# Optimization experiments

Hardware: AMD Instinct MI355X
Metric: run time of the kernel (lower is better)

## Reference

```python
import jax, jax.numpy as jnp
import numpy as np

B, NX, NY, T = 8, 512, 512, 2_000_000


def setup_inputs() -> dict:
    key = jax.random.key(0)
    k1, k2, k3 = jax.random.split(key, 3)
    # regular source grid (flattened row-major: flat = j*NX + i, x varies fastest)
    xs = jnp.linspace(0.0, 1.0, NX, dtype=jnp.float32)
    ys = jnp.linspace(0.0, 1.0, NY, dtype=jnp.float32)
    SX, SY = jnp.meshgrid(xs, ys)  # (NY, NX)
    src_x = SX.reshape(1, -1)
    src_y = SY.reshape(1, -1)
    # target points strictly inside the convex hull (no NaN extrapolation)
    eps = 1e-3
    tgt_x = jax.random.uniform(k1, (1, T), jnp.float32, eps, 1.0 - eps)
    tgt_y = jax.random.uniform(k2, (1, T), jnp.float32, eps, 1.0 - eps)
    x = jax.random.normal(k3, (B, NX * NY, 1), jnp.float32)
    return {"x": x, "src_x": src_x, "src_y": src_y,
            "tgt_x": tgt_x, "tgt_y": tgt_y, "nx": NX, "ny": NY}


def reference(x, src_x, src_y, tgt_x, tgt_y, nx, ny):
    # Linear ND (triangulated) interpolation of x from a regular source grid
    # onto scattered target points. Each grid cell is split along the
    # (i,j)-(i+1,j+1) diagonal; barycentric weights inside each triangle.
    sx = src_x.reshape(-1)
    sy = src_y.reshape(-1)
    tx = tgt_x.reshape(-1)
    ty = tgt_y.reshape(-1)
    x0, x1 = sx.min(), sx.max()
    y0, y1 = sy.min(), sy.max()
    dx = (x1 - x0) / (nx - 1)
    dy = (y1 - y0) / (ny - 1)
    fx = (tx - x0) / dx
    fy = (ty - y0) / dy
    ix = jnp.clip(jnp.floor(fx), 0, nx - 2)
    iy = jnp.clip(jnp.floor(fy), 0, ny - 2)
    u = fx - ix  # local cell coords in [0,1]
    v = fy - iy
    ii = jax.lax.stop_gradient(ix).astype(jnp.int32)
    jj = jax.lax.stop_gradient(iy).astype(jnp.int32)
    base = jj * nx + ii
    i00, i10, i01, i11 = base, base + 1, base + nx, base + nx + 1
    lower = (u + v) <= 1.0  # which triangle of the cell
    idx = jnp.where(lower[:, None],
                    jnp.stack([i00, i10, i01], axis=-1),
                    jnp.stack([i11, i10, i01], axis=-1))  # [t,3]
    w = jnp.where(lower[:, None],
                  jnp.stack([1.0 - u - v, u, v], axis=-1),
                  jnp.stack([u + v - 1.0, 1.0 - v, 1.0 - u], axis=-1))  # [t,3]
    vals = x[:, idx, 0]                      # [b,t,3] gather of triangle vertices
    out = jnp.einsum('btk,tk->bt', vals, w)  # barycentric combination
    return out[..., None]                    # [b,t,1]
```

## Files before the change

### kernel.cpp

```cpp
#include <hip/hip_runtime.h>
#include <hip/hip_fp16.h>


typedef float  f32x4 __attribute__((ext_vector_type(4)));
typedef unsigned int u32x4 __attribute__((ext_vector_type(4)));

__device__ __forceinline__ unsigned pack_h2(float lo, float hi) {
    union { __half2 h2; unsigned u; } cv;
    cv.h2 = __float22half2_rn(make_float2(lo, hi));
    return cv.u;
}

__global__ __launch_bounds__(256) void build_grid16(
    const float* __restrict__ x,
    u32x4* __restrict__ rec,
    int N)
{
    const int p0 = (blockIdx.x * blockDim.x + threadIdx.x) * 4;
    if (p0 + 4 <= N) {
        f32x4 v[8];
        #pragma unroll
        for (int b = 0; b < 8; ++b)
            v[b] = *reinterpret_cast<const f32x4*>(x + (long)b * N + p0);
        #pragma unroll
        for (int k = 0; k < 4; ++k) {
            u32x4 r;
            r[0] = pack_h2(v[0][k], v[1][k]);
            r[1] = pack_h2(v[2][k], v[3][k]);
            r[2] = pack_h2(v[4][k], v[5][k]);
            r[3] = pack_h2(v[6][k], v[7][k]);
            rec[p0 + k] = r;
        }
    } else {
        for (int p = p0; p < N; ++p) {
            u32x4 r;
            r[0] = pack_h2(x[p], x[(long)N + p]);
            r[1] = pack_h2(x[2L * N + p], x[3L * N + p]);
            r[2] = pack_h2(x[4L * N + p], x[5L * N + p]);
            r[3] = pack_h2(x[6L * N + p], x[7L * N + p]);
            rec[p] = r;
        }
    }
}

__device__ __forceinline__ void half8_to_float8(u32x4 u, float* f) {
    union { u32x4 v; __half2 h2[4]; } cv;
    cv.v = u;
    float2 a = __half22float2(cv.h2[0]); f[0] = a.x; f[1] = a.y;
    float2 b = __half22float2(cv.h2[1]); f[2] = b.x; f[3] = b.y;
    float2 c = __half22float2(cv.h2[2]); f[4] = c.x; f[5] = c.y;
    float2 d = __half22float2(cv.h2[3]); f[6] = d.x; f[7] = d.y;
}

#define TPT 4

#define LOAD_TGT(c, tx, ty) do {                                          \
    const int _t0 = (c) * TPT;                                            \
    tx = __builtin_nontemporal_load(                                      \
        reinterpret_cast<const f32x4*>(tgt_x + _t0));                     \
    ty = __builtin_nontemporal_load(                                      \
        reinterpret_cast<const f32x4*>(tgt_y + _t0));                     \
} while (0)

#define GATHER(tx, ty, w0, w1, w2, r0, r1, r2) do {                       \
    _Pragma("unroll")                                                     \
    for (int k = 0; k < TPT; ++k) {                                       \
        float fx = (tx[k] - x0) * rdx;                                    \
        float fy = (ty[k] - y0) * rdy;                                    \
        float ix = fminf(fmaxf(floorf(fx), 0.0f), ixmax);                 \
        float iy = fminf(fmaxf(floorf(fy), 0.0f), iymax);                 \
        float u = fx - ix;                                                \
        float v = fy - iy;                                                \
        bool lower = (u + v) <= 1.0f;                                     \
        int g = (int)iy * nx + (int)ix;                                   \
        w0[k] = lower ? (1.0f - u - v) : (u + v - 1.0f);                  \
        w1[k] = lower ? u : (1.0f - v);                                   \
        w2[k] = lower ? v : (1.0f - u);                                   \
        r0[k] = rec[g + (lower ? 0 : (nx + 1))];                          \
        r1[k] = rec[g + 1];                                               \
        r2[k] = rec[g + nx];                                              \
    }                                                                     \
} while (0)

#define CONSUME(c, w0, w1, w2, r0, r1, r2) do {                           \
    const int _t0 = (c) * TPT;                                            \
    float res[TPT][8];                                                    \
    _Pragma("unroll")                                                     \
    for (int k = 0; k < TPT; ++k) {                                       \
        float f0[8], f1[8], f2[8];                                        \
        half8_to_float8(r0[k], f0);                                       \
        half8_to_float8(r1[k], f1);                                       \
        half8_to_float8(r2[k], f2);                                       \
        _Pragma("unroll")                                                 \
        for (int b = 0; b < 8; ++b)                                       \
            res[k][b] = f0[b] * w0[k] + f1[b] * w1[k] + f2[b] * w2[k];    \
    }                                                                     \
    _Pragma("unroll")                                                     \
    for (int b = 0; b < 8; ++b) {                                         \
        f32x4 r4 = { res[0][b], res[1][b], res[2][b], res[3][b] };        \
        __builtin_nontemporal_store(                                      \
            r4, reinterpret_cast<f32x4*>(out + (long)b * T + _t0));       \
    }                                                                     \
} while (0)

__global__ __launch_bounds__(256, 2) void interp_pipe_kernel(
    const u32x4* __restrict__ rec,
    const float* __restrict__ src_x,
    const float* __restrict__ src_y,
    const float* __restrict__ tgt_x,
    const float* __restrict__ tgt_y,
    const int* __restrict__ nx_p,
    float* __restrict__ out,
    int T, int N)
{
    const int nx = *nx_p;
    const int ny = N / nx;
    const float x0 = src_x[0];
    const float x1 = src_x[nx - 1];
    const float y0 = src_y[0];
    const float y1 = src_y[N - 1];
    const float rdx = (float)(nx - 1) / (x1 - x0);
    const float rdy = (float)(ny - 1) / (y1 - y0);
    const float ixmax = (float)(nx - 2);
    const float iymax = (float)(ny - 2);

    const int nch = T / TPT;
    const int gsz = gridDim.x * blockDim.x;
    const int tid = blockIdx.x * blockDim.x + threadIdx.x;

    {
        const int tail0 = nch * TPT;
        if (tid < T - tail0) {
            const int t = tail0 + tid;
            float fx = (tgt_x[t] - x0) * rdx;
            float fy = (tgt_y[t] - y0) * rdy;
            float ix = fminf(fmaxf(floorf(fx), 0.0f), ixmax);
            float iy = fminf(fmaxf(floorf(fy), 0.0f), iymax);
            float u = fx - ix;
            float v = fy - iy;
            bool lower = (u + v) <= 1.0f;
            int g = (int)iy * nx + (int)ix;
            u32x4 q0 = rec[g + (lower ? 0 : (nx + 1))];
            u32x4 q1 = rec[g + 1];
            u32x4 q2 = rec[g + nx];
            float w0 = lower ? (1.0f - u - v) : (u + v - 1.0f);
            float w1 = lower ? u : (1.0f - v);
            float w2 = lower ? v : (1.0f - u);
            float f0[8], f1[8], f2[8];
            half8_to_float8(q0, f0);
            half8_to_float8(q1, f1);
            half8_to_float8(q2, f2);
            for (int b = 0; b < 8; ++b)
                out[(long)b * T + t] = f0[b] * w0 + f1[b] * w1 + f2[b] * w2;
        }
    }

    int cCur = tid;
    if (cCur >= nch) return;
    int cNxt = cCur + gsz;
    int cPre = cNxt + gsz;

    f32x4 txA, tyA, txB, tyB;
    float wA0[TPT], wA1[TPT], wA2[TPT];
    float wB0[TPT], wB1[TPT], wB2[TPT];
    u32x4 rA0[TPT], rA1[TPT], rA2[TPT];
    u32x4 rB0[TPT], rB1[TPT], rB2[TPT];

    LOAD_TGT(cCur, txA, tyA);
    bool haveNxt = (cNxt < nch);
    if (haveNxt) LOAD_TGT(cNxt, txB, tyB);
    GATHER(txA, tyA, wA0, wA1, wA2, rA0, rA1, rA2);

    while (true) {
        if (!haveNxt) { CONSUME(cCur, wA0, wA1, wA2, rA0, rA1, rA2); break; }
        if (cPre < nch) LOAD_TGT(cPre, txA, tyA);
        GATHER(txB, tyB, wB0, wB1, wB2, rB0, rB1, rB2);
        CONSUME(cCur, wA0, wA1, wA2, rA0, rA1, rA2);
        cCur = cNxt; cNxt = cPre; cPre += gsz;
        haveNxt = (cNxt < nch);
        if (!haveNxt) { CONSUME(cCur, wB0, wB1, wB2, rB0, rB1, rB2); break; }
        if (cPre < nch) LOAD_TGT(cPre, txB, tyB);
        GATHER(txA, tyA, wA0, wA1, wA2, rA0, rA1, rA2);
        CONSUME(cCur, wB0, wB1, wB2, rB0, rB1, rB2);
        cCur = cNxt; cNxt = cPre; cPre += gsz;
        haveNxt = (cNxt < nch);
    }
}

__global__ __launch_bounds__(256) void interp_fallback_kernel(
    const float* __restrict__ x,
    const float* __restrict__ src_x,
    const float* __restrict__ src_y,
    const float* __restrict__ tgt_x,
    const float* __restrict__ tgt_y,
    const int* __restrict__ nx_p,
    float* __restrict__ out,
    int T, int N, int B)
{
    const int nx = *nx_p;
    const int ny = N / nx;
    const float x0 = src_x[0];
    const float x1 = src_x[nx - 1];
    const float y0 = src_y[0];
    const float y1 = src_y[N - 1];
    const float rdx = (float)(nx - 1) / (x1 - x0);
    const float rdy = (float)(ny - 1) / (y1 - y0);

    const int t = blockIdx.x * blockDim.x + threadIdx.x;
    if (t >= T) return;
    float fx = (tgt_x[t] - x0) * rdx;
    float fy = (tgt_y[t] - y0) * rdy;
    float ix = fminf(fmaxf(floorf(fx), 0.0f), (float)(nx - 2));
    float iy = fminf(fmaxf(floorf(fy), 0.0f), (float)(ny - 2));
    float u = fx - ix;
    float v = fy - iy;
    int base = (int)iy * nx + (int)ix;
    bool lower = (u + v) <= 1.0f;
    int   i0 = lower ? base : (base + nx + 1);
    int   i1 = base + 1;
    int   i2 = base + nx;
    float w0 = lower ? (1.0f - u - v) : (u + v - 1.0f);
    float w1 = lower ? u : (1.0f - v);
    float w2 = lower ? v : (1.0f - u);
    for (int b = 0; b < B; ++b) {
        const float* xb = x + (long)b * N;
        out[(long)b * T + t] = xb[i0] * w0 + xb[i1] * w1 + xb[i2] * w2;
    }
}

extern "C" void kernel_launch(void* const* d_in, const int* in_sizes, int n_in,
                              void* d_out, int out_size, void* d_ws, size_t ws_size,
                              hipStream_t stream) {
    const float* x     = (const float*)d_in[0];
    const float* src_x = (const float*)d_in[1];
    const float* src_y = (const float*)d_in[2];
    const float* tgt_x = (const float*)d_in[3];
    const float* tgt_y = (const float*)d_in[4];
    const int*   nx_p  = (const int*)d_in[5];
    float* out = (float*)d_out;

    const int N = in_sizes[1];
    const int T = in_sizes[3];
    const int B = in_sizes[0] / N;

    const size_t rec_bytes = (size_t)N * 16;

    if (B == 8 && ws_size >= rec_bytes) {
        u32x4* rec = (u32x4*)d_ws;
        {
            const int block = 256;
            const int grid = ((N + 3) / 4 + block - 1) / block;
            build_grid16<<<grid, block, 0, stream>>>(x, rec, N);
        }
        {
            const int nch = T / TPT;
            int grid = (nch + 255) / 256;
            if (grid > 512) grid = 512;
            if (grid < 1) grid = 1;
            interp_pipe_kernel<<<grid, 256, 0, stream>>>(
                rec, src_x, src_y, tgt_x, tgt_y, nx_p, out, T, N);
        }
    } else {
        const int block = 256;
        const int grid = (T + block - 1) / block;
        interp_fallback_kernel<<<grid, block, 0, stream>>>(
            x, src_x, src_y, tgt_x, tgt_y, nx_p, out, T, N, B);
    }
}
```

Before: 129.3 us.

## Store fp16 grid records in 2x2 quad-interleaved layout for gather locality

The packed fp16 grid records are rebuilt so each pair of rows is interleaved column by column: the (i,j), (i,j+1), (i+1,j) and (i+1,j+1) records of a 2x2 quad sit next to each other. The interpolation kernel's index math is rewritten to map cell coordinates to the new slots. The goal is for the three triangle-vertex gathers per target to usually fall in one cache line instead of two lines a full row apart, which cuts cache-line traffic in the gather-bound loop. In exchange, index arithmetic gets a little heavier, and the build kernel now does narrower, strided float2 loads.

Result: no change. 130.8 us (+1.1%).

```diff
diff --git a/kernel.cpp b/kernel.cpp
--- a/kernel.cpp
+++ b/kernel.cpp
@@ -11,35 +11,65 @@
     return cv.u;
 }
 
-__global__ __launch_bounds__(256) void build_grid16(
+__device__ __forceinline__ u32x4 pack8(const float* v) {
+    u32x4 r;
+    r[0] = pack_h2(v[0], v[1]);
+    r[1] = pack_h2(v[2], v[3]);
+    r[2] = pack_h2(v[4], v[5]);
+    r[3] = pack_h2(v[6], v[7]);
+    return r;
+}
+
+__global__ __launch_bounds__(256) void build_grid_quad(
     const float* __restrict__ x,
     u32x4* __restrict__ rec,
+    const int* __restrict__ nx_p,
     int N)
 {
-    const int p0 = (blockIdx.x * blockDim.x + threadIdx.x) * 4;
-    if (p0 + 4 <= N) {
-        f32x4 v[8];
-        #pragma unroll
-        for (int b = 0; b < 8; ++b)
-            v[b] = *reinterpret_cast<const f32x4*>(x + (long)b * N + p0);
-        #pragma unroll
-        for (int k = 0; k < 4; ++k) {
-            u32x4 r;
-            r[0] = pack_h2(v[0][k], v[1][k]);
-            r[1] = pack_h2(v[2][k], v[3][k]);
-            r[2] = pack_h2(v[4][k], v[5][k]);
-            r[3] = pack_h2(v[6][k], v[7][k]);
-            rec[p0 + k] = r;
+    const int nx = *nx_p;
+    const int ny = N / nx;
+    const int qx = (nx + 1) >> 1;
+    const int qy = (ny + 1) >> 1;
+    const int nq = qx * qy;
+    const int q = blockIdx.x * blockDim.x + threadIdx.x;
+    if (q >= nq) return;
+    const int qi = q % qx;
+    const int qj = q / qx;
+    const int i = qi << 1;
+    const int j = qj << 1;
+    const bool i1 = (i + 1 < nx);
+    const bool j1 = (j + 1 < ny);
+    const bool vec2 = ((nx & 1) == 0);
+    const long base = (long)j * nx + i;
+
+    float a0[8], a1[8], b0[8], b1[8];
+    #pragma unroll
+    for (int b = 0; b < 8; ++b) {
+        const float* xb = x + (long)b * N;
+        if (i1 && vec2) {
+            float2 t = *reinterpret_cast<const float2*>(xb + base);
+            a0[b] = t.x; a1[b] = t.y;
+        } else {
+            a0[b] = xb[base];
+            a1[b] = i1 ? xb[base + 1] : 0.0f;
         }
-    } else {
-        for (int p = p0; p < N; ++p) {
-            u32x4 r;
-            r[0] = pack_h2(x[p], x[(long)N + p]);
-            r[1] = pack_h2(x[2L * N + p], x[3L * N + p]);
-            r[2] = pack_h2(x[4L * N + p], x[5L * N + p]);
-            r[3] = pack_h2(x[6L * N + p], x[7L * N + p]);
-            rec[p] = r;
-        }
+        if (j1) {
+            if (i1 && vec2) {
+                float2 t = *reinterpret_cast<const float2*>(xb + base + nx);
+                b0[b] = t.x; b1[b] = t.y;
+            } else {
+                b0[b] = xb[base + nx];
+                b1[b] = i1 ? xb[base + nx + 1] : 0.0f;
+            }
+        } else { b0[b] = 0.0f; b1[b] = 0.0f; }
+    }
+
+    const long s = ((long)qj * nx + i) * 2;
+    rec[s] = pack8(a0);
+    if (j1) rec[s + 1] = pack8(b0);
+    if (i1) {
+        rec[s + 2] = pack8(a1);
+        if (j1) rec[s + 3] = pack8(b1);
     }
 }
 
@@ -72,13 +102,15 @@
         float u = fx - ix;                                                \
         float v = fy - iy;                                                \
         bool lower = (u + v) <= 1.0f;                                     \
-        int g = (int)iy * nx + (int)ix;                                   \
+        int i0 = (int)ix, j0 = (int)iy;                                   \
+        int sA = (j0 >> 1) * nx2 + (i0 << 1) + (j0 & 1);                  \
+        int sC = sA + ((j0 & 1) ? (nx2 - 1) : 1);                         \
         w0[k] = lower ? (1.0f - u - v) : (u + v - 1.0f);                  \
         w1[k] = lower ? u : (1.0f - v);                                   \
         w2[k] = lower ? v : (1.0f - u);                                   \
-        r0[k] = rec[g + (lower ? 0 : (nx + 1))];                          \
-        r1[k] = rec[g + 1];                                               \
-        r2[k] = rec[g + nx];                                              \
+        r0[k] = rec[lower ? sA : (sC + 2)];                               \
+        r1[k] = rec[sA + 2];                                              \
+        r2[k] = rec[sC];                                                  \
     }                                                                     \
 } while (0)
 
@@ -115,6 +147,7 @@
 {
     const int nx = *nx_p;
     const int ny = N / nx;
+    const int nx2 = nx * 2;
     const float x0 = src_x[0];
     const float x1 = src_x[nx - 1];
     const float y0 = src_y[0];
@@ -139,10 +172,12 @@
             float u = fx - ix;
             float v = fy - iy;
             bool lower = (u + v) <= 1.0f;
-            int g = (int)iy * nx + (int)ix;
-            u32x4 q0 = rec[g + (lower ? 0 : (nx + 1))];
-            u32x4 q1 = rec[g + 1];
-            u32x4 q2 = rec[g + nx];
+            int i0 = (int)ix, j0 = (int)iy;
+            int sA = (j0 >> 1) * nx2 + (i0 << 1) + (j0 & 1);
+            int sC = sA + ((j0 & 1) ? (nx2 - 1) : 1);
+            u32x4 q0 = rec[lower ? sA : (sC + 2)];
+            u32x4 q1 = rec[sA + 2];
+            u32x4 q2 = rec[sC];
             float w0 = lower ? (1.0f - u - v) : (u + v - 1.0f);
             float w1 = lower ? u : (1.0f - v);
             float w2 = lower ? v : (1.0f - u);
@@ -243,14 +278,14 @@
     const int T = in_sizes[3];
     const int B = in_sizes[0] / N;
 
-    const size_t rec_bytes = (size_t)N * 16;
+    const size_t rec_bytes = (size_t)N * 2 * 16;
 
     if (B == 8 && ws_size >= rec_bytes) {
         u32x4* rec = (u32x4*)d_ws;
         {
             const int block = 256;
-            const int grid = ((N + 3) / 4 + block - 1) / block;
-            build_grid16<<<grid, block, 0, stream>>>(x, rec, N);
+            const int grid = (N / 2 + block - 1) / block;
+            build_grid_quad<<<grid, block, 0, stream>>>(x, rec, nx_p, N);
         }
         {
             const int nch = T / TPT;
```
